# Performance work log

Hardware: AMD Instinct MI355X
Metric: run time of the kernel (lower is better)

## Reference

```python
import jax, jax.numpy as jnp
import numpy as np

N_NODES = 100000
N_EDGES = 1600000
IN_FEATS = 64
N_CLASSES = 64


def setup_inputs() -> dict:
    key = jax.random.key(0)
    k1, k2, k3, k4, k5 = jax.random.split(key, 5)
    feat = jax.random.normal(k1, (N_NODES, IN_FEATS), dtype=jnp.float32)
    edge_row = jnp.sort(jax.random.randint(k2, (N_EDGES,), 0, N_NODES))
    edge_col = jax.random.randint(k3, (N_EDGES,), 0, N_NODES)
    # values of the cached normalized adjacency power (all positive, ~1/deg scale)
    edge_val = jax.random.uniform(k4, (N_EDGES,), dtype=jnp.float32) / 16.0
    # nn.Linear(in_feats, n_classes): weight [C, F] (xavier), bias zeros
    limit = float(np.sqrt(6.0 / (IN_FEATS + N_CLASSES)))
    W = jax.random.uniform(k5, (N_CLASSES, IN_FEATS), dtype=jnp.float32,
                           minval=-limit, maxval=limit)
    b = jnp.zeros((N_CLASSES,), dtype=jnp.float32)
    return {"feat": feat, "edge_row": edge_row, "edge_col": edge_col,
            "edge_val": edge_val, "W": W, "b": b}


def reference(feat, edge_row, edge_col, edge_val, W, b):
    # SpMM: h = A_pre @ feat, A_pre given as COO (edge_row, edge_col, edge_val)
    msg = edge_val[:, None] * feat[edge_col]          # [E, F] gather + scale
    h = jax.ops.segment_sum(msg, edge_row, num_segments=N_NODES)  # [N, F]
    # fc: Linear(in_feats -> n_classes), norm=None so no normalization
    return h @ W.T + b                                 # [N, C]
```

## Files before the change

kernel.cpp:

```cpp
#include <hip/hip_runtime.h>
#include <hip/hip_bf16.h>

typedef __attribute__((ext_vector_type(8))) short short8;
typedef __attribute__((ext_vector_type(4))) float f32x4;

__device__ __forceinline__ unsigned short f2bf(float x) {
    unsigned int u = __float_as_uint(x);
    unsigned int lsb = (u >> 16) & 1u;
    u += 0x7fffu + lsb;
    return (unsigned short)(u >> 16);
}

__device__ __forceinline__ float bf2f(unsigned int b16) {
    return __uint_as_float(b16 << 16);
}

__device__ __forceinline__ short8 pack8(f32x4 a, f32x4 b) {
    short8 r;
    r[0] = (short)f2bf(a.x); r[1] = (short)f2bf(a.y);
    r[2] = (short)f2bf(a.z); r[3] = (short)f2bf(a.w);
    r[4] = (short)f2bf(b.x); r[5] = (short)f2bf(b.y);
    r[6] = (short)f2bf(b.z); r[7] = (short)f2bf(b.w);
    return r;
}

__global__ __launch_bounds__(256) void k_init(const float* __restrict__ bias,
                                              float* __restrict__ out, long total4) {
    long i4 = (long)blockIdx.x * 256 + threadIdx.x;
    if (i4 < total4) {
        const f32x4* b4 = (const f32x4*)bias;
        ((f32x4*)out)[i4] = b4[i4 & 15];
    }
}

__global__ __launch_bounds__(256) void k_setup(const float* __restrict__ feat,
                                               const float* __restrict__ W,
                                               const float* __restrict__ bias,
                                               unsigned short* __restrict__ G,
                                               float* __restrict__ out,
                                               int N, int gblocks) {
    if ((int)blockIdx.x >= gblocks) {
        long i4 = (long)(blockIdx.x - gblocks) * 256 + threadIdx.x;
        long total4 = (long)N * 16;
        if (i4 < total4) {
            const f32x4* b4 = (const f32x4*)bias;
            ((f32x4*)out)[i4] = b4[i4 & 15];
        }
        return;
    }

    int wave = blockIdx.x * 4 + (threadIdx.x >> 6);
    int lane = threadIdx.x & 63;
    int m0 = wave * 16;
    if (m0 >= N) return;
    int n = lane & 15;
    int quad = lane >> 4;

    short8 bf[4][2];
#pragma unroll
    for (int ct = 0; ct < 4; ++ct)
#pragma unroll
        for (int ks = 0; ks < 2; ++ks) {
            const f32x4* wp = (const f32x4*)(W + (size_t)(ct * 16 + n) * 64 + ks * 32 + quad * 8);
            f32x4 w0 = wp[0];
            f32x4 w1 = wp[1];
            bf[ct][ks] = pack8(w0, w1);
        }

    int mrow = m0 + n; if (mrow >= N) mrow = N - 1;
    short8 af[2];
#pragma unroll
    for (int ks = 0; ks < 2; ++ks) {
        const f32x4* ap = (const f32x4*)(feat + (size_t)mrow * 64 + ks * 32 + quad * 8);
        f32x4 a0 = __builtin_nontemporal_load(ap);
        f32x4 a1 = __builtin_nontemporal_load(ap + 1);
        af[ks] = pack8(a0, a1);
    }

    f32x4 acc[4];
#pragma unroll
    for (int ct = 0; ct < 4; ++ct) {
        acc[ct] = (f32x4){0.f, 0.f, 0.f, 0.f};
#pragma unroll
        for (int ks = 0; ks < 2; ++ks)
            acc[ct] = __builtin_amdgcn_mfma_f32_16x16x32_bf16(af[ks], bf[ct][ks], acc[ct], 0, 0, 0);
    }

#pragma unroll
    for (int ct = 0; ct < 4; ++ct)
#pragma unroll
        for (int r = 0; r < 4; ++r) {
            int rowm = m0 + quad * 4 + r;
            if (rowm < N)
                G[(size_t)rowm * 64 + ct * 16 + n] = f2bf(acc[ct][r]);
        }
}

__global__ __launch_bounds__(256) void k_spmm(const unsigned short* __restrict__ G,
                                              const int* __restrict__ erow,
                                              const int* __restrict__ ecol,
                                              const float* __restrict__ evalv,
                                              const float* __restrict__ bias,
                                              float* __restrict__ out, int E) {
    int wave = blockIdx.x * 4 + (threadIdx.x >> 6);
    int lane = threadIdx.x & 63;
    long base0 = (long)wave * 128;
    if (base0 >= E) return;

    float blane = bias[lane];
    int cur;
    float acc = 0.f;
    bool first = true;

    if (base0 + 128 <= E) {
        long i0 = base0 + lane;
        int rv[2], cv[2], vv[2];
        rv[0] = __builtin_nontemporal_load(erow + i0);
        cv[0] = __builtin_nontemporal_load(ecol + i0);
        vv[0] = __float_as_int(__builtin_nontemporal_load(evalv + i0));
        rv[1] = __builtin_nontemporal_load(erow + i0 + 64);
        cv[1] = __builtin_nontemporal_load(ecol + i0 + 64);
        vv[1] = __float_as_int(__builtin_nontemporal_load(evalv + i0 + 64));

        cur = __builtin_amdgcn_readlane(rv[0], 0);

        unsigned g[2][16];
#pragma unroll
        for (int u = 0; u < 16; ++u) {
            int c = __builtin_amdgcn_readlane(cv[0], u);
            g[0][u] = G[((size_t)(unsigned)c << 6) | (unsigned)lane];
        }
#pragma unroll
        for (int j = 0; j < 8; ++j) {
            if (j < 7) {
                int chp = (j + 1) >> 2, jop = ((j + 1) & 3) * 16;
#pragma unroll
                for (int u = 0; u < 16; ++u) {
                    int c = __builtin_amdgcn_readlane(cv[chp], jop + u);
                    g[(j + 1) & 1][u] = G[((size_t)(unsigned)c << 6) | (unsigned)lane];
                }
            }
            int ch = j >> 2, jo = (j & 3) * 16;
#pragma unroll
            for (int u = 0; u < 16; ++u) {
                int r = __builtin_amdgcn_readlane(rv[ch], jo + u);
                float v = __int_as_float(__builtin_amdgcn_readlane(vv[ch], jo + u));
                if (r != cur) {
                    if (first) {
                        atomicAdd(out + ((size_t)(unsigned)cur << 6) + lane, acc);
                        first = false;
                    } else {
                        out[((size_t)(unsigned)cur << 6) + lane] = blane + acc;
                    }
                    acc = 0.f;
                    cur = r;
                }
                acc = fmaf(v, bf2f(g[j & 1][u]), acc);
            }
        }
    } else {
        cur = __builtin_amdgcn_readfirstlane(erow[base0]);
        long e1 = E;
        for (long e = base0; e < e1; ++e) {
            int r = erow[e];
            int c = ecol[e];
            float v = evalv[e];
            float gg = bf2f(G[((size_t)(unsigned)c << 6) | (unsigned)lane]);
            if (r != cur) {
                if (first) {
                    atomicAdd(out + ((size_t)(unsigned)cur << 6) + lane, acc);
                    first = false;
                } else {
                    out[((size_t)(unsigned)cur << 6) + lane] = blane + acc;
                }
                acc = 0.f;
                cur = r;
            }
            acc = fmaf(v, gg, acc);
        }
    }

    atomicAdd(out + ((size_t)(unsigned)cur << 6) + lane, acc);
}

__global__ __launch_bounds__(256) void k_fused(const float* __restrict__ feat,
                                               const int* __restrict__ erow,
                                               const int* __restrict__ ecol,
                                               const float* __restrict__ evalv,
                                               const float* __restrict__ W,
                                               float* __restrict__ out,
                                               int E, int epw) {
    __shared__ float Wt[64 * 64];
    for (int i = threadIdx.x; i < 4096; i += 256) {
        int c = i >> 6, f = i & 63;
        Wt[f * 64 + c] = W[i];
    }
    __syncthreads();

    int wave = blockIdx.x * 4 + (threadIdx.x >> 6);
    int lane = threadIdx.x & 63;
    long e0 = (long)wave * epw;
    if (e0 >= E) return;
    long e1 = e0 + epw; if (e1 > E) e1 = E;

    int cur = erow[e0];
    float acc = 0.f;
    for (long e = e0; e < e1; ++e) {
        int r = erow[e];
        int c = ecol[e];
        float v = evalv[e];
        float g = feat[((size_t)c << 6) | lane];
        if (r != cur) {
            float res = 0.f;
#pragma unroll
            for (int f = 0; f < 64; ++f)
                res += __shfl(acc, f, 64) * Wt[f * 64 + lane];
            atomicAdd(out + ((size_t)cur << 6) + lane, res);
            acc = 0.f;
            cur = r;
        }
        acc += v * g;
    }
    {
        float res = 0.f;
#pragma unroll
        for (int f = 0; f < 64; ++f)
            res += __shfl(acc, f, 64) * Wt[f * 64 + lane];
        atomicAdd(out + ((size_t)cur << 6) + lane, res);
    }
}

extern "C" void kernel_launch(void* const* d_in, const int* in_sizes, int n_in,
                              void* d_out, int out_size, void* d_ws, size_t ws_size,
                              hipStream_t stream) {
    const float* feat  = (const float*)d_in[0];
    const int*   erow  = (const int*)d_in[1];
    const int*   ecol  = (const int*)d_in[2];
    const float* evalv = (const float*)d_in[3];
    const float* W     = (const float*)d_in[4];
    const float* bias  = (const float*)d_in[5];
    float* out = (float*)d_out;

    int N = in_sizes[0] / 64;
    int E = in_sizes[1];

    size_t need = (size_t)N * 64 * sizeof(unsigned short);
    if (ws_size >= need) {
        unsigned short* G = (unsigned short*)d_ws;
        int tiles = (N + 15) / 16;
        int gblocks = (tiles + 3) / 4;
        long total4 = (long)N * 16;
        int iblocks = (int)((total4 + 255) / 256);
        k_setup<<<gblocks + iblocks, 256, 0, stream>>>(feat, W, bias, G, out, N, gblocks);

        int nwaves = (E + 127) / 128;
        int nblocks = (nwaves + 3) / 4;
        k_spmm<<<nblocks, 256, 0, stream>>>(G, erow, ecol, evalv, bias, out, E);
    } else {
        long total4 = (long)N * 16;
        k_init<<<(int)((total4 + 255) / 256), 256, 0, stream>>>(bias, out, total4);
        int epw = (E + 8191) / 8192;
        if (epw < 32) epw = 32;
        int nwaves = (E + epw - 1) / epw;
        int nblocks = (nwaves + 3) / 4;
        k_fused<<<nblocks, 256, 0, stream>>>(feat, erow, ecol, evalv, W, out, E, epw);
    }
}
```

Before: 141.6 us.

## Process four edges per wave step with 8-byte bf16 gathers and shuffle reduction

The SpMM kernel is rewritten so that each group of 16 lanes handles one edge and each lane loads four bf16 features in one 8-byte access. A wave therefore covers four edges per step instead of one. Partial sums are combined across the four lane groups with xor shuffles before each row flush, and row changes inside a group of four are handled with a masked loop. Each wave now processes 64 edges instead of 128, doubling the wave count. This trades fewer, wider gather instructions for extra shuffle and flush work and more atomics at wave boundaries.

```diff
diff --git a/kernel.cpp b/kernel.cpp
--- a/kernel.cpp
+++ b/kernel.cpp
@@ -3,6 +3,7 @@
 
 typedef __attribute__((ext_vector_type(8))) short short8;
 typedef __attribute__((ext_vector_type(4))) float f32x4;
+typedef __attribute__((ext_vector_type(2))) unsigned int u32x2;
 
 __device__ __forceinline__ unsigned short f2bf(float x) {
     unsigned int u = __float_as_uint(x);
@@ -104,83 +105,112 @@
                                               float* __restrict__ out, int E) {
     int wave = blockIdx.x * 4 + (threadIdx.x >> 6);
     int lane = threadIdx.x & 63;
-    long base0 = (long)wave * 128;
+    long base0 = (long)wave * 64;
     if (base0 >= E) return;
 
-    float blane = bias[lane];
+    int fb = lane & 15;
+    int q  = lane >> 4;
+    f32x4 b4 = ((const f32x4*)bias)[fb];
+
+    float acc0 = 0.f, acc1 = 0.f, acc2 = 0.f, acc3 = 0.f;
+    bool first = true;
     int cur;
-    float acc = 0.f;
-    bool first = true;
-
-    if (base0 + 128 <= E) {
+
+    auto flush = [&](bool atomic_path) {
+        float t0 = acc0 + __shfl_xor(acc0, 16);
+        float t1 = acc1 + __shfl_xor(acc1, 16);
+        float t2 = acc2 + __shfl_xor(acc2, 16);
+        float t3 = acc3 + __shfl_xor(acc3, 16);
+        t0 += __shfl_xor(t0, 32);
+        t1 += __shfl_xor(t1, 32);
+        t2 += __shfl_xor(t2, 32);
+        t3 += __shfl_xor(t3, 32);
+        if (lane < 16) {
+            float* p = out + ((size_t)(unsigned)cur << 6) + ((unsigned)fb << 2);
+            if (atomic_path) {
+                atomicAdd(p + 0, t0);
+                atomicAdd(p + 1, t1);
+                atomicAdd(p + 2, t2);
+                atomicAdd(p + 3, t3);
+            } else {
+                f32x4 o = {b4.x + t0, b4.y + t1, b4.z + t2, b4.w + t3};
+                *(f32x4*)p = o;
+            }
+        }
+        acc0 = acc1 = acc2 = acc3 = 0.f;
+    };
+
+    if (base0 + 64 <= E) {
         long i0 = base0 + lane;
-        int rv[2], cv[2], vv[2];
-        rv[0] = __builtin_nontemporal_load(erow + i0);
-        cv[0] = __builtin_nontemporal_load(ecol + i0);
-        vv[0] = __float_as_int(__builtin_nontemporal_load(evalv + i0));
-        rv[1] = __builtin_nontemporal_load(erow + i0 + 64);
-        cv[1] = __builtin_nontemporal_load(ecol + i0 + 64);
-        vv[1] = __float_as_int(__builtin_nontemporal_load(evalv + i0 + 64));
-
-        cur = __builtin_amdgcn_readlane(rv[0], 0);
-
-        unsigned g[2][16];
-#pragma unroll
-        for (int u = 0; u < 16; ++u) {
-            int c = __builtin_amdgcn_readlane(cv[0], u);
-            g[0][u] = G[((size_t)(unsigned)c << 6) | (unsigned)lane];
-        }
-#pragma unroll
-        for (int j = 0; j < 8; ++j) {
-            if (j < 7) {
-                int chp = (j + 1) >> 2, jop = ((j + 1) & 3) * 16;
-#pragma unroll
-                for (int u = 0; u < 16; ++u) {
-                    int c = __builtin_amdgcn_readlane(cv[chp], jop + u);
-                    g[(j + 1) & 1][u] = G[((size_t)(unsigned)c << 6) | (unsigned)lane];
+        int rv = __builtin_nontemporal_load(erow + i0);
+        int cv = __builtin_nontemporal_load(ecol + i0);
+        int vv = __builtin_nontemporal_load((const int*)evalv + i0);
+
+        cur = __builtin_amdgcn_readlane(rv, 0);
+
+        int vq4 = q << 2;
+        unsigned vfb8 = (unsigned)fb << 3;
+
+        u32x2 g[16];
+#pragma unroll
+        for (int k = 0; k < 16; ++k) {
+            int c = __builtin_amdgcn_ds_bpermute(vq4 + 16 * k, cv);
+            unsigned off = ((unsigned)c << 7) + vfb8;
+            g[k] = *(const u32x2*)((const char*)G + off);
+        }
+        __builtin_amdgcn_sched_barrier(0);
+
+#pragma unroll
+        for (int k = 0; k < 16; ++k) {
+            int r0 = __builtin_amdgcn_readlane(rv, 4 * k);
+            int r3 = __builtin_amdgcn_readlane(rv, 4 * k + 3);
+            float vs = __int_as_float(__builtin_amdgcn_ds_bpermute(vq4 + 16 * k, vv));
+            float f0 = __uint_as_float(g[k].x << 16);
+            float f1 = __uint_as_float(g[k].x & 0xffff0000u);
+            float f2 = __uint_as_float(g[k].y << 16);
+            float f3 = __uint_as_float(g[k].y & 0xffff0000u);
+
+            if (r0 == r3) {
+                if (r0 != cur) { flush(first); first = false; cur = r0; }
+                acc0 = fmaf(vs, f0, acc0);
+                acc1 = fmaf(vs, f1, acc1);
+                acc2 = fmaf(vs, f2, acc2);
+                acc3 = fmaf(vs, f3, acc3);
+            } else {
+                int rowsv = __builtin_amdgcn_ds_bpermute(vq4 + 16 * k, rv);
+                int r1 = __builtin_amdgcn_readlane(rv, 4 * k + 1);
+                int r2 = __builtin_amdgcn_readlane(rv, 4 * k + 2);
+                int rr = r0;
+                while (true) {
+                    if (rr != cur) { flush(first); first = false; cur = rr; }
+                    float vm = (rowsv == rr) ? vs : 0.f;
+                    acc0 = fmaf(vm, f0, acc0);
+                    acc1 = fmaf(vm, f1, acc1);
+                    acc2 = fmaf(vm, f2, acc2);
+                    acc3 = fmaf(vm, f3, acc3);
+                    if (rr == r3) break;
+                    rr = (r1 > rr) ? r1 : ((r2 > rr) ? r2 : r3);
                 }
             }
-            int ch = j >> 2, jo = (j & 3) * 16;
-#pragma unroll
-            for (int u = 0; u < 16; ++u) {
-                int r = __builtin_amdgcn_readlane(rv[ch], jo + u);
-                float v = __int_as_float(__builtin_amdgcn_readlane(vv[ch], jo + u));
-                if (r != cur) {
-                    if (first) {
-                        atomicAdd(out + ((size_t)(unsigned)cur << 6) + lane, acc);
-                        first = false;
-                    } else {
-                        out[((size_t)(unsigned)cur << 6) + lane] = blane + acc;
-                    }
-                    acc = 0.f;
-                    cur = r;
-                }
-                acc = fmaf(v, bf2f(g[j & 1][u]), acc);
-            }
         }
     } else {
-        cur = __builtin_amdgcn_readfirstlane(erow[base0]);
-        long e1 = E;
-        for (long e = base0; e < e1; ++e) {
+        cur = erow[base0];
+        unsigned vfb8 = (unsigned)fb << 3;
+        for (long e = base0; e < (long)E; ++e) {
             int r = erow[e];
             int c = ecol[e];
             float v = evalv[e];
-            float gg = bf2f(G[((size_t)(unsigned)c << 6) | (unsigned)lane]);
-            if (r != cur) {
-                if (first) {
-                    atomicAdd(out + ((size_t)(unsigned)cur << 6) + lane, acc);
-                    first = false;
-                } else {
-                    out[((size_t)(unsigned)cur << 6) + lane] = blane + acc;
-                }
-                acc = 0.f;
-                cur = r;
-            }
-            acc = fmaf(v, gg, acc);
-        }
-    }
-
-    atomicAdd(out + ((size_t)(unsigned)cur << 6) + lane, acc);
+            u32x2 gg = *(const u32x2*)((const char*)G + (((unsigned)c << 7) + vfb8));
+            if (r != cur) { flush(first); first = false; cur = r; }
+            float vm = (q == 0) ? v : 0.f;
+            acc0 = fmaf(vm, __uint_as_float(gg.x << 16), acc0);
+            acc1 = fmaf(vm, __uint_as_float(gg.x & 0xffff0000u), acc1);
+            acc2 = fmaf(vm, __uint_as_float(gg.y << 16), acc2);
+            acc3 = fmaf(vm, __uint_as_float(gg.y & 0xffff0000u), acc3);
+        }
+    }
+
+    flush(true);
 }
 
 __global__ __launch_bounds__(256) void k_fused(const float* __restrict__ feat,
@@ -253,7 +283,7 @@
         int iblocks = (int)((total4 + 255) / 256);
         k_setup<<<gblocks + iblocks, 256, 0, stream>>>(feat, W, bias, G, out, N, gblocks);
 
-        int nwaves = (E + 127) / 128;
+        int nwaves = (E + 63) / 64;
         int nblocks = (nwaves + 3) / 4;
         k_spmm<<<nblocks, 256, 0, stream>>>(G, erow, ecol, evalv, bias, out, E);
     } else {
```

After: 166.6 us. 17.7% more time.

## Split projected features into 16-column planes and process four edges per wave step

Applied to the files above, without the earlier changes.

The projected bf16 feature matrix G is stored as four planes of 16 columns each, one per feature group. Each SpMM block now handles one group, with the block index interleaved so the groups of one edge range run on neighbouring blocks. Inside a wave, lanes are split into four quarters that gather rows for four different edges at once using ds_bpermute. Partial sums are reduced across quarters with shuffles before each output row is written. This raises gather parallelism and makes each gather 32 bytes instead of 128, but the edge index and value arrays are now read four times and there is extra shuffle work and branching where a row boundary falls inside a group of four edges.

```diff
diff --git a/kernel.cpp b/kernel.cpp
--- a/kernel.cpp
+++ b/kernel.cpp
@@ -9,10 +9,6 @@
     unsigned int lsb = (u >> 16) & 1u;
     u += 0x7fffu + lsb;
     return (unsigned short)(u >> 16);
-}
-
-__device__ __forceinline__ float bf2f(unsigned int b16) {
-    return __uint_as_float(b16 << 16);
 }
 
 __device__ __forceinline__ short8 pack8(f32x4 a, f32x4 b) {
@@ -86,13 +82,14 @@
             acc[ct] = __builtin_amdgcn_mfma_f32_16x16x32_bf16(af[ks], bf[ct][ks], acc[ct], 0, 0, 0);
     }
 
+    size_t pstride = (size_t)N * 16;
 #pragma unroll
     for (int ct = 0; ct < 4; ++ct)
 #pragma unroll
         for (int r = 0; r < 4; ++r) {
             int rowm = m0 + quad * 4 + r;
             if (rowm < N)
-                G[(size_t)rowm * 64 + ct * 16 + n] = f2bf(acc[ct][r]);
+                G[(size_t)ct * pstride + (size_t)rowm * 16 + n] = f2bf(acc[ct][r]);
         }
 }
 
@@ -101,86 +98,97 @@
                                               const int* __restrict__ ecol,
                                               const float* __restrict__ evalv,
                                               const float* __restrict__ bias,
-                                              float* __restrict__ out, int E) {
-    int wave = blockIdx.x * 4 + (threadIdx.x >> 6);
+                                              float* __restrict__ out, int E, int N) {
+    int b = blockIdx.x;
+    int fg  = (b & 7) >> 1;
+    int sub = (b >> 3) * 2 + (b & 1);
+    int wavein = threadIdx.x >> 6;
     int lane = threadIdx.x & 63;
-    long base0 = (long)wave * 128;
+    long base0 = ((long)sub * 4 + wavein) * 128;
     if (base0 >= E) return;
 
-    float blane = bias[lane];
-    int cur;
+    int fb = lane & 15;
+    int q  = lane >> 4;
+    const unsigned short* plane = G + (size_t)fg * ((size_t)N * 16);
+    float blane = bias[fg * 16 + fb];
+
     float acc = 0.f;
     bool first = true;
+    int cur;
+
+    auto flush = [&](bool atomic_path) {
+        float t = acc + __shfl_xor(acc, 16);
+        t += __shfl_xor(t, 32);
+        if (lane < 16) {
+            float* p = out + ((size_t)(unsigned)cur << 6) + (unsigned)(fg * 16 + lane);
+            if (atomic_path) atomicAdd(p, t);
+            else *p = blane + t;
+        }
+        acc = 0.f;
+    };
 
     if (base0 + 128 <= E) {
         long i0 = base0 + lane;
         int rv[2], cv[2], vv[2];
         rv[0] = __builtin_nontemporal_load(erow + i0);
         cv[0] = __builtin_nontemporal_load(ecol + i0);
-        vv[0] = __float_as_int(__builtin_nontemporal_load(evalv + i0));
+        vv[0] = __builtin_nontemporal_load((const int*)evalv + i0);
         rv[1] = __builtin_nontemporal_load(erow + i0 + 64);
         cv[1] = __builtin_nontemporal_load(ecol + i0 + 64);
-        vv[1] = __float_as_int(__builtin_nontemporal_load(evalv + i0 + 64));
+        vv[1] = __builtin_nontemporal_load((const int*)evalv + i0 + 64);
 
         cur = __builtin_amdgcn_readlane(rv[0], 0);
 
-        unsigned g[2][16];
-#pragma unroll
-        for (int u = 0; u < 16; ++u) {
-            int c = __builtin_amdgcn_readlane(cv[0], u);
-            g[0][u] = G[((size_t)(unsigned)c << 6) | (unsigned)lane];
-        }
-#pragma unroll
-        for (int j = 0; j < 8; ++j) {
-            if (j < 7) {
-                int chp = (j + 1) >> 2, jop = ((j + 1) & 3) * 16;
-#pragma unroll
-                for (int u = 0; u < 16; ++u) {
-                    int c = __builtin_amdgcn_readlane(cv[chp], jop + u);
-                    g[(j + 1) & 1][u] = G[((size_t)(unsigned)c << 6) | (unsigned)lane];
+        int vq4 = q << 2;
+
+        unsigned short gbuf[32];
+#pragma unroll
+        for (int k = 0; k < 32; ++k) {
+            int c = __builtin_amdgcn_ds_bpermute(vq4 + 16 * (k & 15), cv[k >> 4]);
+            gbuf[k] = plane[(size_t)(unsigned)c * 16 + fb];
+        }
+        __builtin_amdgcn_sched_barrier(0);
+
+#pragma unroll
+        for (int k = 0; k < 32; ++k) {
+            int ch = k >> 4;
+            int i4 = (k & 15) * 4;
+            int r0 = __builtin_amdgcn_readlane(rv[ch], i4);
+            int r3 = __builtin_amdgcn_readlane(rv[ch], i4 + 3);
+            float vs = __int_as_float(__builtin_amdgcn_ds_bpermute(vq4 + i4 * 4, vv[ch]));
+            float f = __uint_as_float((unsigned)gbuf[k] << 16);
+
+            if (r0 == r3) {
+                if (r0 != cur) { flush(first); first = false; cur = r0; }
+                acc = fmaf(vs, f, acc);
+            } else {
+                int rowsv = __builtin_amdgcn_ds_bpermute(vq4 + i4 * 4, rv[ch]);
+                int r1 = __builtin_amdgcn_readlane(rv[ch], i4 + 1);
+                int r2 = __builtin_amdgcn_readlane(rv[ch], i4 + 2);
+                int rr = r0;
+                while (true) {
+                    if (rr != cur) { flush(first); first = false; cur = rr; }
+                    float vm = (rowsv == rr) ? vs : 0.f;
+                    acc = fmaf(vm, f, acc);
+                    if (rr == r3) break;
+                    rr = (r1 > rr) ? r1 : ((r2 > rr) ? r2 : r3);
                 }
             }
-            int ch = j >> 2, jo = (j & 3) * 16;
-#pragma unroll
-            for (int u = 0; u < 16; ++u) {
-                int r = __builtin_amdgcn_readlane(rv[ch], jo + u);
-                float v = __int_as_float(__builtin_amdgcn_readlane(vv[ch], jo + u));
-                if (r != cur) {
-                    if (first) {
-                        atomicAdd(out + ((size_t)(unsigned)cur << 6) + lane, acc);
-                        first = false;
-                    } else {
-                        out[((size_t)(unsigned)cur << 6) + lane] = blane + acc;
-                    }
-                    acc = 0.f;
-                    cur = r;
-                }
-                acc = fmaf(v, bf2f(g[j & 1][u]), acc);
-            }
         }
     } else {
-        cur = __builtin_amdgcn_readfirstlane(erow[base0]);
-        long e1 = E;
-        for (long e = base0; e < e1; ++e) {
+        cur = erow[base0];
+        for (long e = base0; e < (long)E; ++e) {
             int r = erow[e];
             int c = ecol[e];
             float v = evalv[e];
-            float gg = bf2f(G[((size_t)(unsigned)c << 6) | (unsigned)lane]);
-            if (r != cur) {
-                if (first) {
-                    atomicAdd(out + ((size_t)(unsigned)cur << 6) + lane, acc);
-                    first = false;
-                } else {
-                    out[((size_t)(unsigned)cur << 6) + lane] = blane + acc;
-                }
-                acc = 0.f;
-                cur = r;
-            }
-            acc = fmaf(v, gg, acc);
-        }
-    }
-
-    atomicAdd(out + ((size_t)(unsigned)cur << 6) + lane, acc);
+            float f = __uint_as_float((unsigned)plane[(size_t)(unsigned)c * 16 + fb] << 16);
+            if (r != cur) { flush(first); first = false; cur = r; }
+            float vm = (q == 0) ? v : 0.f;
+            acc = fmaf(vm, f, acc);
+        }
+    }
+
+    flush(true);
 }
 
 __global__ __launch_bounds__(256) void k_fused(const float* __restrict__ feat,
@@ -253,9 +261,10 @@
         int iblocks = (int)((total4 + 255) / 256);
         k_setup<<<gblocks + iblocks, 256, 0, stream>>>(feat, W, bias, G, out, N, gblocks);
 
-        int nwaves = (E + 127) / 128;
-        int nblocks = (nwaves + 3) / 4;
-        k_spmm<<<nblocks, 256, 0, stream>>>(G, erow, ecol, evalv, bias, out, E);
+        int nwpf = (E + 127) / 128;
+        int bpf  = (nwpf + 3) / 4;
+        int noct = (bpf + 1) / 2;
+        k_spmm<<<noct * 8, 256, 0, stream>>>(G, erow, ecol, evalv, bias, out, E, N);
     } else {
         long total4 = (long)N * 16;
         k_init<<<(int)((total4 + 255) / 256), 256, 0, stream>>>(bias, out, total4);
```

Result: slower. 187.3 us (+32.3%).

## Process two edges per wave step with half-waves loading 4-byte bf16 pairs

Applied to the files above, without the earlier changes.

The SpMM kernel is restructured so each half-wave handles a different edge and each lane loads two bf16 features (4 bytes) instead of one. Partial sums from the two halves are combined with a cross-half shuffle when a row ends. Row boundaries are found up front with ballot bitmasks, and gathers are triple-buffered over 256 edges per wave instead of 128. The aim is to halve the number of gather instructions and raise bytes per load, at the cost of more complex flush logic, shuffles, and fewer waves in flight.

```diff
diff --git a/kernel.cpp b/kernel.cpp
--- a/kernel.cpp
+++ b/kernel.cpp
@@ -9,10 +9,6 @@
     unsigned int lsb = (u >> 16) & 1u;
     u += 0x7fffu + lsb;
     return (unsigned short)(u >> 16);
-}
-
-__device__ __forceinline__ float bf2f(unsigned int b16) {
-    return __uint_as_float(b16 << 16);
 }
 
 __device__ __forceinline__ short8 pack8(f32x4 a, f32x4 b) {
@@ -104,83 +100,158 @@
                                               float* __restrict__ out, int E) {
     int wave = blockIdx.x * 4 + (threadIdx.x >> 6);
     int lane = threadIdx.x & 63;
-    long base0 = (long)wave * 128;
+    long base0 = (long)wave * 256;
     if (base0 >= E) return;
 
-    float blane = bias[lane];
+    int l5 = lane & 31;
+    bool hi = lane >= 32;
+    unsigned voff = (unsigned)l5 * 4u;
+    int vb4 = hi ? 4 : 0;
+    const char* Gb = (const char*)G;
+    float2 b2 = ((const float2*)bias)[l5];
+
+    float acc0 = 0.f, acc1 = 0.f;
+    bool first = true;
     int cur;
-    float acc = 0.f;
-    bool first = true;
-
-    if (base0 + 128 <= E) {
+
+    auto flush_atomic = [&]() {
+        float t0 = acc0 + __shfl_xor(acc0, 32);
+        float t1 = acc1 + __shfl_xor(acc1, 32);
+        if (lane < 32) {
+            float* p = out + ((size_t)(unsigned)cur << 6) + (unsigned)(l5 * 2);
+            atomicAdd(p, t0);
+            atomicAdd(p + 1, t1);
+        }
+        acc0 = 0.f; acc1 = 0.f;
+    };
+    auto flush = [&]() {
+        if (first) { flush_atomic(); first = false; return; }
+        float t0 = acc0 + __shfl_xor(acc0, 32);
+        float t1 = acc1 + __shfl_xor(acc1, 32);
+        if (lane < 32) {
+            float* p = out + ((size_t)(unsigned)cur << 6) + (unsigned)(l5 * 2);
+            float2 o; o.x = b2.x + t0; o.y = b2.y + t1;
+            *(float2*)p = o;
+        }
+        acc0 = 0.f; acc1 = 0.f;
+    };
+
+    if (base0 + 256 <= E) {
         long i0 = base0 + lane;
-        int rv[2], cv[2], vv[2];
-        rv[0] = __builtin_nontemporal_load(erow + i0);
-        cv[0] = __builtin_nontemporal_load(ecol + i0);
-        vv[0] = __float_as_int(__builtin_nontemporal_load(evalv + i0));
-        rv[1] = __builtin_nontemporal_load(erow + i0 + 64);
-        cv[1] = __builtin_nontemporal_load(ecol + i0 + 64);
-        vv[1] = __float_as_int(__builtin_nontemporal_load(evalv + i0 + 64));
-
+        int rv[4], cv[4], vvv[4];
+#pragma unroll
+        for (int c = 0; c < 4; ++c) {
+            rv[c]  = __builtin_nontemporal_load(erow + i0 + 64 * c);
+            cv[c]  = __builtin_nontemporal_load(ecol + i0 + 64 * c);
+            vvv[c] = __builtin_nontemporal_load((const int*)evalv + i0 + 64 * c);
+        }
         cur = __builtin_amdgcn_readlane(rv[0], 0);
 
-        unsigned g[2][16];
-#pragma unroll
-        for (int u = 0; u < 16; ++u) {
-            int c = __builtin_amdgcn_readlane(cv[0], u);
-            g[0][u] = G[((size_t)(unsigned)c << 6) | (unsigned)lane];
-        }
-#pragma unroll
-        for (int j = 0; j < 8; ++j) {
-            if (j < 7) {
-                int chp = (j + 1) >> 2, jop = ((j + 1) & 3) * 16;
-#pragma unroll
-                for (int u = 0; u < 16; ++u) {
-                    int c = __builtin_amdgcn_readlane(cv[chp], jop + u);
-                    g[(j + 1) & 1][u] = G[((size_t)(unsigned)c << 6) | (unsigned)lane];
+        unsigned long long bm[4];
+#pragma unroll
+        for (int c = 0; c < 4; ++c) {
+            int rn = __shfl_down(rv[c], 1);
+            unsigned long long m = __ballot(rv[c] != rn) & 0x7fffffffffffffffULL;
+            int r63 = __builtin_amdgcn_readlane(rv[c], 63);
+            int n0  = (c < 3) ? __builtin_amdgcn_readlane(rv[c + 1], 0) : (r63 + 1);
+            if (r63 != n0) m |= 0x8000000000000000ULL;
+            bm[c] = m;
+        }
+
+        unsigned gbuf[3][16];
+
+#define SPMM_ISSUE(GI, SLOT) do {                                              \
+    _Pragma("unroll")                                                          \
+    for (int k_ = 0; k_ < 16; ++k_) {                                          \
+        const int p_ = (GI) * 16 + k_;                                         \
+        const int c_ = p_ >> 5;                                                \
+        const int pj_ = p_ & 31;                                               \
+        int idx_ = vb4 + 8 * pj_;                                              \
+        int colv_ = __builtin_amdgcn_ds_bpermute(idx_, cv[c_]);                \
+        unsigned off_ = ((unsigned)colv_ << 7) + voff;                         \
+        gbuf[SLOT][k_] = *(const unsigned*)(Gb + off_);                        \
+    } } while (0)
+
+        SPMM_ISSUE(0, 0);
+        SPMM_ISSUE(1, 1);
+
+#pragma unroll
+        for (int g = 0; g < 8; ++g) {
+            if (g < 6) SPMM_ISSUE(g + 2, (g + 2) % 3);
+            __builtin_amdgcn_sched_barrier(0);
+
+#pragma unroll
+            for (int k = 0; k < 16; ++k) {
+                const int p  = g * 16 + k;
+                const int c  = p >> 5;
+                const int pj = p & 31;
+                int idx = vb4 + 8 * pj;
+                float vs = __int_as_float(__builtin_amdgcn_ds_bpermute(idx, vvv[c]));
+                unsigned u = gbuf[g % 3][k];
+                float flo = __uint_as_float(u << 16);
+                float fhi = __uint_as_float(u & 0xffff0000u);
+                int A = (pj > 0) ? (int)((bm[c] >> (2 * pj - 1)) & 1ULL)
+                      : (c > 0)  ? (int)((bm[c - 1] >> 63) & 1ULL) : 0;
+                int B = (int)((bm[c] >> (2 * pj)) & 1ULL);
+                if ((A | B) == 0) {
+                    acc0 = fmaf(vs, flo, acc0);
+                    acc1 = fmaf(vs, fhi, acc1);
+                } else if (B == 0) {
+                    flush();
+                    cur = __builtin_amdgcn_readlane(rv[c], 2 * pj);
+                    acc0 = fmaf(vs, flo, acc0);
+                    acc1 = fmaf(vs, fhi, acc1);
+                } else {
+                    if (A) {
+                        flush();
+                        cur = __builtin_amdgcn_readlane(rv[c], 2 * pj);
+                    }
+                    float vsl = hi ? 0.f : vs;
+                    acc0 = fmaf(vsl, flo, acc0);
+                    acc1 = fmaf(vsl, fhi, acc1);
+                    flush();
+                    cur = __builtin_amdgcn_readlane(rv[c], 2 * pj + 1);
+                    float vsh = hi ? vs : 0.f;
+                    acc0 = fmaf(vsh, flo, acc0);
+                    acc1 = fmaf(vsh, fhi, acc1);
                 }
             }
-            int ch = j >> 2, jo = (j & 3) * 16;
-#pragma unroll
-            for (int u = 0; u < 16; ++u) {
-                int r = __builtin_amdgcn_readlane(rv[ch], jo + u);
-                float v = __int_as_float(__builtin_amdgcn_readlane(vv[ch], jo + u));
-                if (r != cur) {
-                    if (first) {
-                        atomicAdd(out + ((size_t)(unsigned)cur << 6) + lane, acc);
-                        first = false;
-                    } else {
-                        out[((size_t)(unsigned)cur << 6) + lane] = blane + acc;
-                    }
-                    acc = 0.f;
-                    cur = r;
-                }
-                acc = fmaf(v, bf2f(g[j & 1][u]), acc);
+        }
+#undef SPMM_ISSUE
+    } else {
+        cur = erow[base0];
+        for (long e = base0; e < (long)E; e += 2) {
+            int r0 = erow[e];
+            int c0 = ecol[e];
+            float v0 = evalv[e];
+            bool has1 = (e + 1 < (long)E);
+            int r1 = has1 ? erow[e + 1] : r0;
+            int c1 = has1 ? ecol[e + 1] : c0;
+            float v1 = has1 ? evalv[e + 1] : 0.f;
+            int csel = hi ? c1 : c0;
+            float vs = hi ? v1 : v0;
+            unsigned off = ((unsigned)csel << 7) + voff;
+            unsigned u = *(const unsigned*)(Gb + off);
+            float flo = __uint_as_float(u << 16);
+            float fhi = __uint_as_float(u & 0xffff0000u);
+            if (r0 != cur) { flush(); cur = r0; }
+            if (r1 == r0) {
+                acc0 = fmaf(vs, flo, acc0);
+                acc1 = fmaf(vs, fhi, acc1);
+            } else {
+                float vsl = hi ? 0.f : vs;
+                acc0 = fmaf(vsl, flo, acc0);
+                acc1 = fmaf(vsl, fhi, acc1);
+                flush();
+                cur = r1;
+                float vsh = hi ? vs : 0.f;
+                acc0 = fmaf(vsh, flo, acc0);
+                acc1 = fmaf(vsh, fhi, acc1);
             }
         }
-    } else {
-        cur = __builtin_amdgcn_readfirstlane(erow[base0]);
-        long e1 = E;
-        for (long e = base0; e < e1; ++e) {
-            int r = erow[e];
-            int c = ecol[e];
-            float v = evalv[e];
-            float gg = bf2f(G[((size_t)(unsigned)c << 6) | (unsigned)lane]);
-            if (r != cur) {
-                if (first) {
-                    atomicAdd(out + ((size_t)(unsigned)cur << 6) + lane, acc);
-                    first = false;
-                } else {
-                    out[((size_t)(unsigned)cur << 6) + lane] = blane + acc;
-                }
-                acc = 0.f;
-                cur = r;
-            }
-            acc = fmaf(v, gg, acc);
-        }
-    }
-
-    atomicAdd(out + ((size_t)(unsigned)cur << 6) + lane, acc);
+    }
+
+    flush_atomic();
 }
 
 __global__ __launch_bounds__(256) void k_fused(const float* __restrict__ feat,
@@ -253,7 +324,7 @@
         int iblocks = (int)((total4 + 255) / 256);
         k_setup<<<gblocks + iblocks, 256, 0, stream>>>(feat, W, bias, G, out, N, gblocks);
 
-        int nwaves = (E + 127) / 128;
+        int nwaves = (E + 255) / 256;
         int nblocks = (nwaves + 3) / 4;
         k_spmm<<<nblocks, 256, 0, stream>>>(G, erow, ecol, evalv, bias, out, E);
     } else {
```

After: 166.9 us. 17.9% more time.
